# Performance work log

Hardware: AMD Instinct MI355X
Metric: run time of the kernel (lower is better)

The kernel has to match this reference:

```python
import jax, jax.numpy as jnp
import numpy as np

MULT = 32       # multiplicity per irrep type (both input and output)
N = 262144      # number of nodes/examples
LS = (0, 1, 2, 3)  # irrep degrees -> block sizes 2l+1 = 1,3,5,7


def setup_inputs() -> dict:
    key = jax.random.key(0)
    keys = jax.random.split(key, 2 * len(LS))
    inp = {}
    for j, l in enumerate(LS):
        m = 2 * l + 1
        inp[f"x{l}"] = jax.random.normal(keys[2 * j], (N, MULT, m), dtype=jnp.float32)
        inp[f"W{l}"] = jax.random.normal(keys[2 * j + 1], (MULT, MULT, m), dtype=jnp.float32)
    return inp


def reference(x0, x1, x2, x3, W0, W1, W2, W3):
    # Block-diagonal equivariant linear: for each irrep type l,
    # out[n, o, m] = sum_i W_l[o, i, m] * x_l[n, i, m]
    # (elementwise in m within each 2l+1 block, summed over input multiplicity i).
    outs = [
        jnp.einsum("nim,oim->nom", x, W)
        for x, W in ((x0, W0), (x1, W1), (x2, W2), (x3, W3))
    ]
    # Concatenate flattened irrep blocks -> [N, MULT*(1+3+5+7)] = [N, 512]
    return jnp.concatenate([o.reshape(o.shape[0], -1) for o in outs], axis=-1)
```

## Files before the change

### kernel.cpp

```cpp
#include <hip/hip_runtime.h>
#include <hip/hip_fp16.h>


#define NTH 512
#define TN  32

typedef _Float16 f16x8 __attribute__((ext_vector_type(8)));
typedef float    f32x4 __attribute__((ext_vector_type(4)));

#define LGKM0_BAR() do { asm volatile("s_waitcnt lgkmcnt(0)" ::: "memory"); \
                         __builtin_amdgcn_s_barrier(); } while (0)

template<int M_, int PB>
__device__ __forceinline__ void stageW(const float* __restrict__ src,
                                       __half* __restrict__ dst, int tid)
{
    #pragma unroll
    for (int it = 0; it < (256 * M_ + NTH - 1) / NTH; ++it) {
        const int f = tid + it * NTH;
        if (f < 256 * M_) {
            float4 v = ((const float4*)src)[f];
            const float vf[4] = {v.x, v.y, v.z, v.w};
            const int e0 = 4 * f;
            #pragma unroll
            for (int k = 0; k < 4; ++k) {
                const int e = e0 + k;
                const int o = e / (32 * M_);
                const int r = e - o * (32 * M_);
                const int i = r / M_, mi = r - i * M_;
                dst[(PB + mi) * 1280 + o * 40 + i] = __float2half(vf[k]);
            }
        }
    }
}

template<int M_, int PB>
__device__ __forceinline__ void mkoff(int tloc, int* offk)
{
    const int e0    = 4 * tloc;
    const int nodel = e0 / (32 * M_);
    const int r0    = e0 - nodel * (32 * M_);
    #pragma unroll
    for (int k = 0; k < 4; ++k) {
        const int ii = (r0 + k) / M_, mi = (r0 + k) - ii * M_;
        offk[k] = (PB + mi) * 1280 + nodel * 40 + ii;
    }
}

__device__ __forceinline__ void plane_info(int p, int& Mm, int& BASE, int& MI)
{
    if (p == 0)     { Mm = 1; BASE = 0;   MI = 0;     }
    else if (p < 4) { Mm = 3; BASE = 32;  MI = p - 1; }
    else if (p < 9) { Mm = 5; BASE = 128; MI = p - 4; }
    else            { Mm = 7; BASE = 288; MI = p - 9; }
}

__global__ __launch_bounds__(NTH, 4) void eqlin(
    const float* __restrict__ x0, const float* __restrict__ x1,
    const float* __restrict__ x2, const float* __restrict__ x3,
    const float* __restrict__ w0, const float* __restrict__ w1,
    const float* __restrict__ w2, const float* __restrict__ w3,
    float* __restrict__ out, int n_tiles)
{
    __shared__ __align__(16) __half XT[20480];
    __shared__ __align__(16) __half OC[16640];
    const int tid  = threadIdx.x;
    const int wave = tid >> 6;
    const int lane = tid & 63;

    int thrg, Mg, offk[4];
    const float* xb;
    bool isM1 = false;
    if (tid < 32)       { thrg = 32;  Mg = 1; xb = x0; mkoff<1, 0>(tid,       offk); isM1 = true; }
    else if (tid < 128) { thrg = 96;  Mg = 3; xb = x1; mkoff<3, 1>(tid - 32,  offk); }
    else if (tid < 288) { thrg = 160; Mg = 5; xb = x2; mkoff<5, 4>(tid - 128, offk); }
    else                { thrg = 224; Mg = 7; xb = x3; mkoff<7, 9>(tid - 288, offk); }
    const int  tloc    = (tid < 32) ? tid : (tid < 128) ? tid - 32 : (tid < 288) ? tid - 128 : tid - 288;
    const long jstride = 4L * thrg;
    const long tstride = (long)gridDim.x * 1024L * Mg;

    const float* srcp = xb + (long)blockIdx.x * (1024L * Mg) + 4 * tloc;
    float4 pf[8];
    #pragma unroll
    for (int j = 0; j < 8; ++j)
        pf[j] = *(const float4*)(srcp + j * jstride);

    stageW<1, 0>(w0, XT, tid);
    stageW<3, 1>(w1, XT, tid);
    stageW<5, 4>(w2, XT, tid);
    stageW<7, 9>(w3, XT, tid);

    const int lrow = lane & 15;
    const int lk8  = (lane >> 4) * 8;
    const int crow = (lane >> 4) * 4;

    LGKM0_BAR();
    f16x8 Wf[2][2];
    {
        const __half* wb = XT + (wave * 2) * 1280 + lrow * 40 + lk8;
        Wf[0][0] = *(const f16x8*)wb;
        Wf[0][1] = *(const f16x8*)(wb + 640);
        Wf[1][0] = *(const f16x8*)(wb + 1280);
        Wf[1][1] = *(const f16x8*)(wb + 1920);
    }
    LGKM0_BAR();

    int Mm0, BASE0, MI0, Mm1, BASE1, MI1;
    plane_info(wave * 2,     Mm0, BASE0, MI0);
    plane_info(wave * 2 + 1, Mm1, BASE1, MI1);

    long prev_node0 = -1;
    for (int t = blockIdx.x; t < n_tiles; t += gridDim.x) {
        const long node0 = (long)t * TN;

        #pragma unroll
        for (int j = 0; j < 8; ++j) {
            const float4 v = pf[j];
            const int jb = j * 160;
            if (isM1) {
                __half2* p = (__half2*)&XT[offk[0] + jb];
                p[0] = __floats2half2_rn(v.x, v.y);
                p[1] = __floats2half2_rn(v.z, v.w);
            } else {
                XT[offk[0] + jb] = __float2half(v.x);
                XT[offk[1] + jb] = __float2half(v.y);
                XT[offk[2] + jb] = __float2half(v.z);
                XT[offk[3] + jb] = __float2half(v.w);
            }
        }
        if (t + (long)gridDim.x < n_tiles) {
            srcp += tstride;
            #pragma unroll
            for (int j = 0; j < 8; ++j)
                pf[j] = *(const float4*)(srcp + j * jstride);
        }
        if (prev_node0 >= 0) {
            float* dst = out + prev_node0 * 512;
            #pragma unroll
            for (int it = 0; it < 4; ++it) {
                const int d0   = 8 * tid + 4096 * it;
                const int node = d0 >> 9, col = d0 & 511;
                uint4 h8 = *(const uint4*)(OC + node * 520 + col);
                const __half2* hp = (const __half2*)&h8;
                float2 f0 = __half22float2(hp[0]);
                float2 f1 = __half22float2(hp[1]);
                float2 f2 = __half22float2(hp[2]);
                float2 f3 = __half22float2(hp[3]);
                *(float4*)(dst + d0)     = make_float4(f0.x, f0.y, f1.x, f1.y);
                *(float4*)(dst + d0 + 4) = make_float4(f2.x, f2.y, f3.x, f3.y);
            }
        }

        LGKM0_BAR();

        f32x4 acc[2][2][2] = {};
        #pragma unroll
        for (int pl = 0; pl < 2; ++pl) {
            const int plane = wave * 2 + pl;
            const __half* xp = XT + plane * 1280 + lrow * 40 + lk8;
            f16x8 A0 = *(const f16x8*)xp;
            f16x8 A1 = *(const f16x8*)(xp + 640);
            acc[pl][0][0] = __builtin_amdgcn_mfma_f32_16x16x32_f16(A0, Wf[pl][0], acc[pl][0][0], 0, 0, 0);
            acc[pl][0][1] = __builtin_amdgcn_mfma_f32_16x16x32_f16(A0, Wf[pl][1], acc[pl][0][1], 0, 0, 0);
            acc[pl][1][0] = __builtin_amdgcn_mfma_f32_16x16x32_f16(A1, Wf[pl][0], acc[pl][1][0], 0, 0, 0);
            acc[pl][1][1] = __builtin_amdgcn_mfma_f32_16x16x32_f16(A1, Wf[pl][1], acc[pl][1][1], 0, 0, 0);
        }
        #pragma unroll
        for (int pl = 0; pl < 2; ++pl) {
            const int Mm   = pl ? Mm1   : Mm0;
            const int BASE = pl ? BASE1 : BASE0;
            const int MI   = pl ? MI1   : MI0;
            #pragma unroll
            for (int nh = 0; nh < 2; ++nh)
            #pragma unroll
            for (int oh = 0; oh < 2; ++oh) {
                const int o     = oh * 16 + lrow;
                const int colb  = BASE + o * Mm + MI;
                const int nodeb = nh * 16 + crow;
                #pragma unroll
                for (int r = 0; r < 4; ++r)
                    OC[(nodeb + r) * 520 + colb] = __float2half(acc[pl][nh][oh][r]);
            }
        }

        LGKM0_BAR();
        prev_node0 = node0;
    }

    if (prev_node0 >= 0) {
        float* dst = out + prev_node0 * 512;
        #pragma unroll
        for (int it = 0; it < 4; ++it) {
            const int d0   = 8 * tid + 4096 * it;
            const int node = d0 >> 9, col = d0 & 511;
            uint4 h8 = *(const uint4*)(OC + node * 520 + col);
            const __half2* hp = (const __half2*)&h8;
            float2 f0 = __half22float2(hp[0]);
            float2 f1 = __half22float2(hp[1]);
            float2 f2 = __half22float2(hp[2]);
            float2 f3 = __half22float2(hp[3]);
            *(float4*)(dst + d0)     = make_float4(f0.x, f0.y, f1.x, f1.y);
            *(float4*)(dst + d0 + 4) = make_float4(f2.x, f2.y, f3.x, f3.y);
        }
    }
}

extern "C" void kernel_launch(void* const* d_in, const int* in_sizes, int n_in,
                              void* d_out, int out_size, void* d_ws, size_t ws_size,
                              hipStream_t stream)
{
    long tot = 0;
    for (int i = 0; i < n_in; ++i) tot += in_sizes[i];
    const long N = (tot - 16384) / 512;
    const int  ms[4] = {1, 3, 5, 7};
    const float* xs[4]  = {nullptr, nullptr, nullptr, nullptr};
    const float* wsp[4] = {nullptr, nullptr, nullptr, nullptr};
    for (int i = 0; i < n_in; ++i) {
        const long s = in_sizes[i];
        for (int l = 0; l < 4; ++l) {
            if (s == N * 32 * ms[l])      xs[l]  = (const float*)d_in[i];
            else if (s == 1024L * ms[l])  wsp[l] = (const float*)d_in[i];
        }
    }
    const int n_tiles = (int)(N / TN);
    const int grid = 512;
    hipLaunchKernelGGL(eqlin, dim3(grid), dim3(NTH), 0, stream,
                       xs[0], xs[1], xs[2], xs[3],
                       wsp[0], wsp[1], wsp[2], wsp[3],
                       (float*)d_out, n_tiles);
}
```

Baseline: 210.2 us.

## Swizzle LDS columns per plane, move output store earlier, double grid

Rotates the k-column index in the shared XT buffer by 8*plane (mod 32). The weight staging, input scatter and MFMA fragment reads all use the rotated index, which is meant to spread LDS bank accesses across planes. The global store of the previous tile's output now runs at the top of the loop, before the input scatter, so stores issue earlier. The grid doubles from 512 to 1024 blocks for more parallelism, at the cost of each block staging the weights again and handling fewer tiles to amortize that.

```diff
diff --git a/kernel.cpp b/kernel.cpp
--- a/kernel.cpp
+++ b/kernel.cpp
@@ -28,7 +28,8 @@
                 const int o = e / (32 * M_);
                 const int r = e - o * (32 * M_);
                 const int i = r / M_, mi = r - i * M_;
-                dst[(PB + mi) * 1280 + o * 40 + i] = __float2half(vf[k]);
+                const int p = PB + mi;
+                dst[p * 1280 + o * 40 + ((i + 8 * p) & 31)] = __float2half(vf[k]);
             }
         }
     }
@@ -43,7 +44,8 @@
     #pragma unroll
     for (int k = 0; k < 4; ++k) {
         const int ii = (r0 + k) / M_, mi = (r0 + k) - ii * M_;
-        offk[k] = (PB + mi) * 1280 + nodel * 40 + ii;
+        const int p  = PB + mi;
+        offk[k] = p * 1280 + nodel * 40 + ((ii + 8 * p) & 31);
     }
 }
 
@@ -53,6 +55,24 @@
     else if (p < 4) { Mm = 3; BASE = 32;  MI = p - 1; }
     else if (p < 9) { Mm = 5; BASE = 128; MI = p - 4; }
     else            { Mm = 7; BASE = 288; MI = p - 9; }
+}
+
+__device__ __forceinline__ void store_tile(const __half* __restrict__ OC,
+                                           float* __restrict__ dst, int tid)
+{
+    #pragma unroll
+    for (int it = 0; it < 4; ++it) {
+        const int d0   = 8 * tid + 4096 * it;
+        const int node = d0 >> 9, col = d0 & 511;
+        uint4 h8 = *(const uint4*)(OC + node * 520 + col);
+        const __half2* hp = (const __half2*)&h8;
+        float2 f0 = __half22float2(hp[0]);
+        float2 f1 = __half22float2(hp[1]);
+        float2 f2 = __half22float2(hp[2]);
+        float2 f3 = __half22float2(hp[3]);
+        *(float4*)(dst + d0)     = make_float4(f0.x, f0.y, f1.x, f1.y);
+        *(float4*)(dst + d0 + 4) = make_float4(f2.x, f2.y, f3.x, f3.y);
+    }
 }
 
 __global__ __launch_bounds__(NTH, 4) void eqlin(
@@ -93,25 +113,28 @@
     const int lrow = lane & 15;
     const int lk8  = (lane >> 4) * 8;
     const int crow = (lane >> 4) * 4;
+    const int p0   = wave * 2, p1 = wave * 2 + 1;
+    const int c0   = (lk8 + 8 * p0) & 31;
+    const int c1   = (lk8 + 8 * p1) & 31;
 
     LGKM0_BAR();
     f16x8 Wf[2][2];
-    {
-        const __half* wb = XT + (wave * 2) * 1280 + lrow * 40 + lk8;
-        Wf[0][0] = *(const f16x8*)wb;
-        Wf[0][1] = *(const f16x8*)(wb + 640);
-        Wf[1][0] = *(const f16x8*)(wb + 1280);
-        Wf[1][1] = *(const f16x8*)(wb + 1920);
-    }
+    Wf[0][0] = *(const f16x8*)(XT + p0 * 1280 + lrow * 40 + c0);
+    Wf[0][1] = *(const f16x8*)(XT + p0 * 1280 + (lrow + 16) * 40 + c0);
+    Wf[1][0] = *(const f16x8*)(XT + p1 * 1280 + lrow * 40 + c1);
+    Wf[1][1] = *(const f16x8*)(XT + p1 * 1280 + (lrow + 16) * 40 + c1);
     LGKM0_BAR();
 
     int Mm0, BASE0, MI0, Mm1, BASE1, MI1;
-    plane_info(wave * 2,     Mm0, BASE0, MI0);
-    plane_info(wave * 2 + 1, Mm1, BASE1, MI1);
+    plane_info(p0, Mm0, BASE0, MI0);
+    plane_info(p1, Mm1, BASE1, MI1);
 
     long prev_node0 = -1;
     for (int t = blockIdx.x; t < n_tiles; t += gridDim.x) {
         const long node0 = (long)t * TN;
+
+        if (prev_node0 >= 0)
+            store_tile(OC, out + prev_node0 * 512, tid);
 
         #pragma unroll
         for (int j = 0; j < 8; ++j) {
@@ -134,36 +157,25 @@
             for (int j = 0; j < 8; ++j)
                 pf[j] = *(const float4*)(srcp + j * jstride);
         }
-        if (prev_node0 >= 0) {
-            float* dst = out + prev_node0 * 512;
-            #pragma unroll
-            for (int it = 0; it < 4; ++it) {
-                const int d0   = 8 * tid + 4096 * it;
-                const int node = d0 >> 9, col = d0 & 511;
-                uint4 h8 = *(const uint4*)(OC + node * 520 + col);
-                const __half2* hp = (const __half2*)&h8;
-                float2 f0 = __half22float2(hp[0]);
-                float2 f1 = __half22float2(hp[1]);
-                float2 f2 = __half22float2(hp[2]);
-                float2 f3 = __half22float2(hp[3]);
-                *(float4*)(dst + d0)     = make_float4(f0.x, f0.y, f1.x, f1.y);
-                *(float4*)(dst + d0 + 4) = make_float4(f2.x, f2.y, f3.x, f3.y);
-            }
-        }
 
         LGKM0_BAR();
 
         f32x4 acc[2][2][2] = {};
-        #pragma unroll
-        for (int pl = 0; pl < 2; ++pl) {
-            const int plane = wave * 2 + pl;
-            const __half* xp = XT + plane * 1280 + lrow * 40 + lk8;
-            f16x8 A0 = *(const f16x8*)xp;
-            f16x8 A1 = *(const f16x8*)(xp + 640);
-            acc[pl][0][0] = __builtin_amdgcn_mfma_f32_16x16x32_f16(A0, Wf[pl][0], acc[pl][0][0], 0, 0, 0);
-            acc[pl][0][1] = __builtin_amdgcn_mfma_f32_16x16x32_f16(A0, Wf[pl][1], acc[pl][0][1], 0, 0, 0);
-            acc[pl][1][0] = __builtin_amdgcn_mfma_f32_16x16x32_f16(A1, Wf[pl][0], acc[pl][1][0], 0, 0, 0);
-            acc[pl][1][1] = __builtin_amdgcn_mfma_f32_16x16x32_f16(A1, Wf[pl][1], acc[pl][1][1], 0, 0, 0);
+        {
+            const __half* xp0 = XT + p0 * 1280 + lrow * 40 + c0;
+            const __half* xp1 = XT + p1 * 1280 + lrow * 40 + c1;
+            f16x8 A00 = *(const f16x8*)xp0;
+            f16x8 A01 = *(const f16x8*)(xp0 + 640);
+            f16x8 A10 = *(const f16x8*)xp1;
+            f16x8 A11 = *(const f16x8*)(xp1 + 640);
+            acc[0][0][0] = __builtin_amdgcn_mfma_f32_16x16x32_f16(A00, Wf[0][0], acc[0][0][0], 0, 0, 0);
+            acc[0][0][1] = __builtin_amdgcn_mfma_f32_16x16x32_f16(A00, Wf[0][1], acc[0][0][1], 0, 0, 0);
+            acc[0][1][0] = __builtin_amdgcn_mfma_f32_16x16x32_f16(A01, Wf[0][0], acc[0][1][0], 0, 0, 0);
+            acc[0][1][1] = __builtin_amdgcn_mfma_f32_16x16x32_f16(A01, Wf[0][1], acc[0][1][1], 0, 0, 0);
+            acc[1][0][0] = __builtin_amdgcn_mfma_f32_16x16x32_f16(A10, Wf[1][0], acc[1][0][0], 0, 0, 0);
+            acc[1][0][1] = __builtin_amdgcn_mfma_f32_16x16x32_f16(A10, Wf[1][1], acc[1][0][1], 0, 0, 0);
+            acc[1][1][0] = __builtin_amdgcn_mfma_f32_16x16x32_f16(A11, Wf[1][0], acc[1][1][0], 0, 0, 0);
+            acc[1][1][1] = __builtin_amdgcn_mfma_f32_16x16x32_f16(A11, Wf[1][1], acc[1][1][1], 0, 0, 0);
         }
         #pragma unroll
         for (int pl = 0; pl < 2; ++pl) {
@@ -187,22 +199,8 @@
         prev_node0 = node0;
     }
 
-    if (prev_node0 >= 0) {
-        float* dst = out + prev_node0 * 512;
-        #pragma unroll
-        for (int it = 0; it < 4; ++it) {
-            const int d0   = 8 * tid + 4096 * it;
-            const int node = d0 >> 9, col = d0 & 511;
-            uint4 h8 = *(const uint4*)(OC + node * 520 + col);
-            const __half2* hp = (const __half2*)&h8;
-            float2 f0 = __half22float2(hp[0]);
-            float2 f1 = __half22float2(hp[1]);
-            float2 f2 = __half22float2(hp[2]);
-            float2 f3 = __half22float2(hp[3]);
-            *(float4*)(dst + d0)     = make_float4(f0.x, f0.y, f1.x, f1.y);
-            *(float4*)(dst + d0 + 4) = make_float4(f2.x, f2.y, f3.x, f3.y);
-        }
-    }
+    if (prev_node0 >= 0)
+        store_tile(OC, out + prev_node0 * 512, tid);
 }
 
 extern "C" void kernel_launch(void* const* d_in, const int* in_sizes, int n_in,
@@ -223,7 +221,7 @@
         }
     }
     const int n_tiles = (int)(N / TN);
-    const int grid = 512;
+    const int grid = 1024;
     hipLaunchKernelGGL(eqlin, dim3(grid), dim3(NTH), 0, stream,
                        xs[0], xs[1], xs[2], xs[3],
                        wsp[0], wsp[1], wsp[2], wsp[3],
```

Result: slower. 218.2 us (+3.8%).
